# Performance work log

Hardware: AMD Instinct MI355X
Metric: run time of the kernel (lower is better)

Reference implementation:

```python
import jax, jax.numpy as jnp
import numpy as np

B, S, D = 2, 2048, 7168
R, H, VD = 1024, 16, 128
QK_HD = R // H            # 64, per-head latent q/k dim
SCALE = float(np.sqrt(D // H))  # self.scale = d_heads ** 0.5 = sqrt(448)


def setup_inputs() -> dict:
    key = jax.random.key(0)
    ks = jax.random.split(key, 6)
    return {
        "x":   jax.random.normal(ks[0], (B, S, D), dtype=jnp.float32),
        "Wq":  jax.random.normal(ks[1], (R, D), dtype=jnp.float32) * 0.02,
        "Wkv": jax.random.normal(ks[2], (R, D), dtype=jnp.float32) * 0.02,
        "Wvb": jax.random.normal(ks[3], (H * VD, R), dtype=jnp.float32) * 0.02,
        "Wo":  jax.random.normal(ks[4], (D, H * VD), dtype=jnp.float32) * 0.02,
        "bo":  jnp.zeros((D,), dtype=jnp.float32),
    }


def reference(x, Wq, Wkv, Wvb, Wo, bo):
    b, s, d = x.shape
    # low-rank compressed projections (torch Linear: y = x @ W.T)
    q_lat  = x @ Wq.T            # [B,S,R] compressed query
    kv_lat = x @ Wkv.T           # [B,S,R] compressed KV latent (shared K)
    q = q_lat.reshape(b, s, H, QK_HD)    # [B,S,H,64]
    k = kv_lat.reshape(b, s, H, QK_HD)   # [B,S,H,64]
    # up-project values from latent
    v = (kv_lat @ Wvb.T).reshape(b, s, H, VD)  # [B,S,H,128]
    # scaled causal attention in latent head space
    scores = jnp.einsum("bqhd,bkhd->bhqk", q, k) / SCALE  # [B,H,S,S]
    causal = jnp.tril(jnp.ones((s, s), dtype=bool))
    scores = jnp.where(causal, scores, jnp.finfo(scores.dtype).min)
    attn = jax.nn.softmax(scores, axis=-1)
    out = jnp.einsum("bhqk,bkhd->bqhd", attn, v).reshape(b, s, H * VD)
    return out @ Wo.T + bo       # [B,S,D]
```

## Files before the change

kernel.cpp:

```cpp
#include <hip/hip_runtime.h>
#include <hip/hip_bf16.h>

typedef __bf16 bf16_t;
typedef __attribute__((ext_vector_type(8))) __bf16 bf16x8;
typedef __attribute__((ext_vector_type(4))) __bf16 bf16x4;
typedef __attribute__((ext_vector_type(4))) float f32x4;

#define B_ 2
#define S_ 2048
#define D_ 7168
#define R_ 1024
#define H_ 16
#define VD_ 128
#define MROWS 4096
#define NQKV 2048
#define HVD 2048

__device__ __forceinline__ void gload_lds16(const bf16_t* g, bf16_t* l) {
    __builtin_amdgcn_global_load_lds(
        (const __attribute__((address_space(1))) unsigned int*)(g),
        (__attribute__((address_space(3))) unsigned int*)(l),
        16, 0, 0);
}

__global__ __launch_bounds__(256)
void cvt_f32_bf16(const float* __restrict__ src, bf16_t* __restrict__ dst, float scale) {
    size_t i = ((size_t)blockIdx.x * 256 + threadIdx.x) * 4;
    f32x4 v = *(const f32x4*)(src + i);
    bf16x4 o;
    o[0] = (bf16_t)(v[0] * scale);
    o[1] = (bf16_t)(v[1] * scale);
    o[2] = (bf16_t)(v[2] * scale);
    o[3] = (bf16_t)(v[3] * scale);
    *(bf16x4*)(dst + i) = o;
}

template<int OUTF32>
__global__ __launch_bounds__(256)
void gemm_bt(const bf16_t* __restrict__ A, int lda,
             const bf16_t* __restrict__ Bt, int ldb,
             void* __restrict__ Cv, int ldc,
             const float* __restrict__ bias, int K)
{
    __shared__ __align__(16) bf16_t As[128 * 64];
    __shared__ __align__(16) bf16_t Bs[128 * 64];
    const int tid  = threadIdx.x;
    const int lane = tid & 63;
    const int wave = tid >> 6;
    const int tileM = blockIdx.y * 128;
    const int tileN = blockIdx.x * 128;
    const int wr = (wave >> 1) * 64;
    const int wc = (wave & 1) * 64;
    const int r  = lane & 15;
    const int kq = lane >> 4;

    const bf16_t* Ag = A  + (size_t)tileM * lda;
    const bf16_t* Bg = Bt + (size_t)tileN * ldb;

    f32x4 acc[4][4] = {};

    for (int k0 = 0; k0 < K; k0 += 64) {
        #pragma unroll
        for (int i = 0; i < 4; ++i) {
            const int lin  = (i * 256 + tid) * 8;
            const int arow = lin >> 6;
            const int acol = (lin & 63) ^ ((arow & 7) << 3);
            gload_lds16(Ag + (size_t)arow * lda + k0 + acol, As + lin);
            gload_lds16(Bg + (size_t)arow * ldb + k0 + acol, Bs + lin);
        }
        __syncthreads();

        bf16x8 af[4][2], bfr[4][2];
        #pragma unroll
        for (int m = 0; m < 4; ++m)
            #pragma unroll
            for (int kk = 0; kk < 2; ++kk) {
                const int e = (wr + m * 16 + r) * 64 + kk * 32 + kq * 8;
                af[m][kk] = *(const bf16x8*)(As + (e ^ ((r & 7) << 3)));
            }
        #pragma unroll
        for (int n = 0; n < 4; ++n)
            #pragma unroll
            for (int kk = 0; kk < 2; ++kk) {
                const int e = (wc + n * 16 + r) * 64 + kk * 32 + kq * 8;
                bfr[n][kk] = *(const bf16x8*)(Bs + (e ^ ((r & 7) << 3)));
            }
        #pragma unroll
        for (int kk = 0; kk < 2; ++kk)
            #pragma unroll
            for (int m = 0; m < 4; ++m)
                #pragma unroll
                for (int n = 0; n < 4; ++n)
                    acc[m][n] = __builtin_amdgcn_mfma_f32_16x16x32_bf16(af[m][kk], bfr[n][kk], acc[m][n], 0, 0, 0);
        __syncthreads();
    }

    const int orow = tileM + wr + kq * 4;
    const int ocol = tileN + wc + r;
    if (OUTF32) {
        float* C = (float*)Cv;
        #pragma unroll
        for (int n = 0; n < 4; ++n) {
            float bv = bias[ocol + n * 16];
            #pragma unroll
            for (int m = 0; m < 4; ++m)
                #pragma unroll
                for (int j = 0; j < 4; ++j)
                    C[(size_t)(orow + m * 16 + j) * ldc + ocol + n * 16] = acc[m][n][j] + bv;
        }
    } else {
        bf16_t* C = (bf16_t*)Cv;
        #pragma unroll
        for (int m = 0; m < 4; ++m)
            #pragma unroll
            for (int n = 0; n < 4; ++n)
                #pragma unroll
                for (int j = 0; j < 4; ++j)
                    C[(size_t)(orow + m * 16 + j) * ldc + ocol + n * 16] = (bf16_t)acc[m][n][j];
    }
}

__device__ __forceinline__ void attn_qtile(
    const bf16_t* __restrict__ Q, const bf16_t* __restrict__ Kp,
    const bf16_t* __restrict__ Vp, bf16_t* __restrict__ Op,
    bf16_t* __restrict__ P_lds, int qbase, int lane)
{
    const int r  = lane & 15;
    const int kq = lane >> 4;

    bf16x8 qf[2][2];
    #pragma unroll
    for (int m = 0; m < 2; ++m)
        #pragma unroll
        for (int kk = 0; kk < 2; ++kk)
            qf[m][kk] = *(const bf16x8*)(Q + (size_t)(qbase + m * 16 + r) * NQKV + kk * 32 + kq * 8);

    f32x4 o[2][8] = {};
    float mst[2][4], lst[2][4];
    #pragma unroll
    for (int m = 0; m < 2; ++m)
        #pragma unroll
        for (int j = 0; j < 4; ++j) { mst[m][j] = -INFINITY; lst[m][j] = 0.0f; }

    const int nfull  = qbase >> 6;
    const int ntiles = (qbase + 95) >> 6;

    for (int t = 0; t < ntiles; ++t) {
        const int kvb = t * 64;
        f32x4 s[2][4] = {};
        #pragma unroll
        for (int n = 0; n < 4; ++n) {
            bf16x8 kf0 = *(const bf16x8*)(Kp + (size_t)(kvb + n * 16 + r) * NQKV + kq * 8);
            bf16x8 kf1 = *(const bf16x8*)(Kp + (size_t)(kvb + n * 16 + r) * NQKV + 32 + kq * 8);
            #pragma unroll
            for (int m = 0; m < 2; ++m) {
                s[m][n] = __builtin_amdgcn_mfma_f32_16x16x32_bf16(qf[m][0], kf0, s[m][n], 0, 0, 0);
                s[m][n] = __builtin_amdgcn_mfma_f32_16x16x32_bf16(qf[m][1], kf1, s[m][n], 0, 0, 0);
            }
        }
        if (t >= nfull) {
            #pragma unroll
            for (int m = 0; m < 2; ++m)
                #pragma unroll
                for (int n = 0; n < 4; ++n)
                    #pragma unroll
                    for (int j = 0; j < 4; ++j) {
                        int kc = kvb + n * 16 + r;
                        int qr = qbase + m * 16 + kq * 4 + j;
                        if (kc > qr) s[m][n][j] = -1e30f;
                    }
        }
        float mx[2][4];
        #pragma unroll
        for (int m = 0; m < 2; ++m)
            #pragma unroll
            for (int j = 0; j < 4; ++j) {
                float v = fmaxf(fmaxf(s[m][0][j], s[m][1][j]), fmaxf(s[m][2][j], s[m][3][j]));
                #pragma unroll
                for (int d = 1; d < 16; d <<= 1) v = fmaxf(v, __shfl_xor(v, d, 64));
                mx[m][j] = v;
            }
        bool need = false;
        #pragma unroll
        for (int m = 0; m < 2; ++m)
            #pragma unroll
            for (int j = 0; j < 4; ++j) need |= (mx[m][j] > mst[m][j] + 8.0f);
        if (__ballot(need)) {
            #pragma unroll
            for (int m = 0; m < 2; ++m)
                #pragma unroll
                for (int j = 0; j < 4; ++j) {
                    float mnew  = fmaxf(mst[m][j], mx[m][j]);
                    float alpha = __expf(mst[m][j] - mnew);
                    lst[m][j] *= alpha;
                    mst[m][j]  = mnew;
                    #pragma unroll
                    for (int n = 0; n < 8; ++n) o[m][n][j] *= alpha;
                }
        }
        #pragma unroll
        for (int m = 0; m < 2; ++m)
            #pragma unroll
            for (int j = 0; j < 4; ++j) {
                float rs = 0.0f;
                const int row = m * 16 + kq * 4 + j;
                #pragma unroll
                for (int n = 0; n < 4; ++n) {
                    float pv = __expf(s[m][n][j] - mst[m][j]);
                    rs += pv;
                    const int c = (n * 16 + r) ^ ((row & 7) << 3);
                    P_lds[row * 64 + c] = (bf16_t)pv;
                }
                #pragma unroll
                for (int d = 1; d < 16; d <<= 1) rs += __shfl_xor(rs, d, 64);
                lst[m][j] += rs;
            }
        __syncthreads();
        bf16x8 pf[2][2];
        #pragma unroll
        for (int m = 0; m < 2; ++m)
            #pragma unroll
            for (int kk = 0; kk < 2; ++kk) {
                const int e = (m * 16 + r) * 64 + kk * 32 + kq * 8;
                pf[m][kk] = *(const bf16x8*)(P_lds + (e ^ ((r & 7) << 3)));
            }
        #pragma unroll
        for (int n = 0; n < 8; ++n) {
            #pragma unroll
            for (int kk = 0; kk < 2; ++kk) {
                bf16x8 vf = *(const bf16x8*)(Vp + (size_t)(n * 16 + r) * MROWS + kvb + kk * 32 + kq * 8);
                #pragma unroll
                for (int m = 0; m < 2; ++m)
                    o[m][n] = __builtin_amdgcn_mfma_f32_16x16x32_bf16(pf[m][kk], vf, o[m][n], 0, 0, 0);
            }
        }
        __syncthreads();
    }

    #pragma unroll
    for (int m = 0; m < 2; ++m)
        #pragma unroll
        for (int j = 0; j < 4; ++j) {
            float inv = 1.0f / lst[m][j];
            int row = m * 16 + kq * 4 + j;
            #pragma unroll
            for (int n = 0; n < 8; ++n)
                Op[(size_t)(qbase + row) * HVD + n * 16 + r] = (bf16_t)(o[m][n][j] * inv);
        }
}

__global__ __launch_bounds__(64)
void attn_kernel(const bf16_t* __restrict__ qkv, const bf16_t* __restrict__ Vt,
                 bf16_t* __restrict__ O)
{
    __shared__ __align__(16) bf16_t P_lds[32 * 64];
    const int lane = threadIdx.x;
    const int p = blockIdx.x;
    const int h = blockIdx.y;
    const int b = blockIdx.z;

    const bf16_t* Q  = qkv + (size_t)(b * S_) * NQKV + h * 64;
    const bf16_t* Kp = qkv + (size_t)(b * S_) * NQKV + R_ + h * 64;
    const bf16_t* Vp = Vt + (size_t)(h * VD_) * MROWS + b * S_;
    bf16_t* Op = O + (size_t)(b * S_) * HVD + h * VD_;

    attn_qtile(Q, Kp, Vp, Op, P_lds, (63 - p) * 32, lane);
    attn_qtile(Q, Kp, Vp, Op, P_lds, p * 32, lane);
}

extern "C" void kernel_launch(void* const* d_in, const int* in_sizes, int n_in,
                              void* d_out, int out_size, void* d_ws, size_t ws_size,
                              hipStream_t stream) {
    const float* x   = (const float*)d_in[0];
    const float* Wq  = (const float*)d_in[1];
    const float* Wkv = (const float*)d_in[2];
    const float* Wvb = (const float*)d_in[3];
    const float* Wo  = (const float*)d_in[4];
    const float* bo  = (const float*)d_in[5];

    char* oc = (char*)d_out;
    bf16_t* xb     = (bf16_t*)oc;
    bf16_t* Wqkv_b = (bf16_t*)(oc + 58720256);
    char* ws = (char*)d_ws;
    bf16_t* qkv_b  = (bf16_t*)ws;
    bf16_t* Wvb_b  = (bf16_t*)(ws + 16777216);
    bf16_t* Vt_b   = (bf16_t*)(ws + 20971520);
    bf16_t* attn_b = (bf16_t*)(ws + 37748736);
    bf16_t* Wo_b   = (bf16_t*)(ws + 54525952);

    const float inv_scale = 0.047245559f;

    cvt_f32_bf16<<<29360128 / 1024, 256, 0, stream>>>(x,   xb, 1.0f);
    cvt_f32_bf16<<< 7340032 / 1024, 256, 0, stream>>>(Wq,  Wqkv_b, inv_scale);
    cvt_f32_bf16<<< 7340032 / 1024, 256, 0, stream>>>(Wkv, Wqkv_b + 7340032, 1.0f);
    cvt_f32_bf16<<< 2097152 / 1024, 256, 0, stream>>>(Wvb, Wvb_b, 1.0f);
    cvt_f32_bf16<<<14680064 / 1024, 256, 0, stream>>>(Wo,  Wo_b, 1.0f);

    gemm_bt<0><<<dim3(16, 32), 256, 0, stream>>>(xb, D_, Wqkv_b, D_, qkv_b, NQKV, nullptr, D_);
    gemm_bt<0><<<dim3(32, 16), 256, 0, stream>>>(Wvb_b, R_, qkv_b + R_, NQKV, Vt_b, MROWS, nullptr, R_);
    attn_kernel<<<dim3(32, H_, B_), 64, 0, stream>>>(qkv_b, Vt_b, attn_b);
    gemm_bt<1><<<dim3(56, 32), 256, 0, stream>>>(attn_b, HVD, Wo_b, HVD, d_out, D_, bo, HVD);
}
```

Before: 542.0 us.

## Double-buffer GEMM LDS tiles and split attention KV loop across four waves

```diff
diff --git a/kernel.cpp b/kernel.cpp
--- a/kernel.cpp
+++ b/kernel.cpp
@@ -42,8 +42,8 @@
              void* __restrict__ Cv, int ldc,
              const float* __restrict__ bias, int K)
 {
-    __shared__ __align__(16) bf16_t As[128 * 64];
-    __shared__ __align__(16) bf16_t Bs[128 * 64];
+    __shared__ __align__(16) bf16_t As[2][128 * 64];
+    __shared__ __align__(16) bf16_t Bs[2][128 * 64];
     const int tid  = threadIdx.x;
     const int lane = tid & 63;
     const int wave = tid >> 6;
@@ -57,18 +57,36 @@
     const bf16_t* Ag = A  + (size_t)tileM * lda;
     const bf16_t* Bg = Bt + (size_t)tileN * ldb;
 
+    int srow[4], scol[4], slin[4];
+    #pragma unroll
+    for (int i = 0; i < 4; ++i) {
+        slin[i] = (i * 256 + tid) * 8;
+        srow[i] = slin[i] >> 6;
+        scol[i] = (slin[i] & 63) ^ ((srow[i] & 7) << 3);
+    }
+
+    #define ISSUE_TILE(buf, k0)                                                  \
+        {                                                                        \
+            _Pragma("unroll")                                                    \
+            for (int i = 0; i < 4; ++i) {                                        \
+                gload_lds16(Ag + (size_t)srow[i] * lda + (k0) + scol[i], As[buf] + slin[i]); \
+                gload_lds16(Bg + (size_t)srow[i] * ldb + (k0) + scol[i], Bs[buf] + slin[i]); \
+            }                                                                    \
+        }
+
     f32x4 acc[4][4] = {};
-
-    for (int k0 = 0; k0 < K; k0 += 64) {
-        #pragma unroll
-        for (int i = 0; i < 4; ++i) {
-            const int lin  = (i * 256 + tid) * 8;
-            const int arow = lin >> 6;
-            const int acol = (lin & 63) ^ ((arow & 7) << 3);
-            gload_lds16(Ag + (size_t)arow * lda + k0 + acol, As + lin);
-            gload_lds16(Bg + (size_t)arow * ldb + k0 + acol, Bs + lin);
-        }
-        __syncthreads();
+    const int nt = K >> 6;
+
+    ISSUE_TILE(0, 0)
+    ISSUE_TILE(1, 64)
+    asm volatile("s_waitcnt vmcnt(8)" ::: "memory");
+    __builtin_amdgcn_s_barrier();
+    __builtin_amdgcn_sched_barrier(0);
+
+    for (int t = 0; t < nt; ++t) {
+        const int cur = t & 1;
+        const bf16_t* Ab = As[cur];
+        const bf16_t* Bb = Bs[cur];
 
         bf16x8 af[4][2], bfr[4][2];
         #pragma unroll
@@ -76,14 +94,14 @@
             #pragma unroll
             for (int kk = 0; kk < 2; ++kk) {
                 const int e = (wr + m * 16 + r) * 64 + kk * 32 + kq * 8;
-                af[m][kk] = *(const bf16x8*)(As + (e ^ ((r & 7) << 3)));
+                af[m][kk] = *(const bf16x8*)(Ab + (e ^ ((r & 7) << 3)));
             }
         #pragma unroll
         for (int n = 0; n < 4; ++n)
             #pragma unroll
             for (int kk = 0; kk < 2; ++kk) {
                 const int e = (wc + n * 16 + r) * 64 + kk * 32 + kq * 8;
-                bfr[n][kk] = *(const bf16x8*)(Bs + (e ^ ((r & 7) << 3)));
+                bfr[n][kk] = *(const bf16x8*)(Bb + (e ^ ((r & 7) << 3)));
             }
         #pragma unroll
         for (int kk = 0; kk < 2; ++kk)
@@ -92,8 +110,19 @@
                 #pragma unroll
                 for (int n = 0; n < 4; ++n)
                     acc[m][n] = __builtin_amdgcn_mfma_f32_16x16x32_bf16(af[m][kk], bfr[n][kk], acc[m][n], 0, 0, 0);
-        __syncthreads();
-    }
+
+        __builtin_amdgcn_s_barrier();
+        __builtin_amdgcn_sched_barrier(0);
+        if (t + 2 < nt) {
+            ISSUE_TILE(cur, (t + 2) << 6)
+            asm volatile("s_waitcnt vmcnt(8)" ::: "memory");
+        } else {
+            asm volatile("s_waitcnt vmcnt(0)" ::: "memory");
+        }
+        __builtin_amdgcn_s_barrier();
+        __builtin_amdgcn_sched_barrier(0);
+    }
+    #undef ISSUE_TILE
 
     const int orow = tileM + wr + kq * 4;
     const int ocol = tileN + wc + r;
@@ -120,10 +149,15 @@
     }
 }
 
-__device__ __forceinline__ void attn_qtile(
+#define OPAD 132
+
+__device__ __forceinline__ void attn_qtile32(
     const bf16_t* __restrict__ Q, const bf16_t* __restrict__ Kp,
     const bf16_t* __restrict__ Vp, bf16_t* __restrict__ Op,
-    bf16_t* __restrict__ P_lds, int qbase, int lane)
+    bf16_t* __restrict__ P_lds,
+    float* __restrict__ O_acc,
+    float* __restrict__ ml_m, float* __restrict__ ml_l,
+    int qbase, int wave, int lane, int tid)
 {
     const int r  = lane & 15;
     const int kq = lane >> 4;
@@ -145,7 +179,7 @@
     const int nfull  = qbase >> 6;
     const int ntiles = (qbase + 95) >> 6;
 
-    for (int t = 0; t < ntiles; ++t) {
+    for (int t = wave; t < ntiles; t += 4) {
         const int kvb = t * 64;
         f32x4 s[2][4] = {};
         #pragma unroll
@@ -215,7 +249,6 @@
                 for (int d = 1; d < 16; d <<= 1) rs += __shfl_xor(rs, d, 64);
                 lst[m][j] += rs;
             }
-        __syncthreads();
         bf16x8 pf[2][2];
         #pragma unroll
         for (int m = 0; m < 2; ++m)
@@ -234,27 +267,82 @@
                     o[m][n] = __builtin_amdgcn_mfma_f32_16x16x32_bf16(pf[m][kk], vf, o[m][n], 0, 0, 0);
             }
         }
+    }
+
+    if (r == 0) {
+        #pragma unroll
+        for (int m = 0; m < 2; ++m)
+            #pragma unroll
+            for (int j = 0; j < 4; ++j) {
+                const int row = m * 16 + kq * 4 + j;
+                ml_m[wave * 32 + row] = mst[m][j];
+                ml_l[wave * 32 + row] = lst[m][j];
+            }
+    }
+    __syncthreads();
+
+    float scl[2][4];
+    #pragma unroll
+    for (int m = 0; m < 2; ++m)
+        #pragma unroll
+        for (int j = 0; j < 4; ++j) {
+            const int row = m * 16 + kq * 4 + j;
+            float M = fmaxf(fmaxf(ml_m[0 * 32 + row], ml_m[1 * 32 + row]),
+                            fmaxf(ml_m[2 * 32 + row], ml_m[3 * 32 + row]));
+            scl[m][j] = __expf(mst[m][j] - M);
+        }
+
+    #pragma unroll
+    for (int wq = 0; wq < 4; ++wq) {
+        if (wave == wq) {
+            #pragma unroll
+            for (int m = 0; m < 2; ++m)
+                #pragma unroll
+                for (int n = 0; n < 8; ++n)
+                    #pragma unroll
+                    for (int j = 0; j < 4; ++j) {
+                        const int row = m * 16 + kq * 4 + j;
+                        const int idx = row * OPAD + n * 16 + r;
+                        float v = o[m][n][j] * scl[m][j];
+                        if (wq == 0) O_acc[idx] = v;
+                        else         O_acc[idx] += v;
+                    }
+        }
         __syncthreads();
     }
 
-    #pragma unroll
-    for (int m = 0; m < 2; ++m)
-        #pragma unroll
-        for (int j = 0; j < 4; ++j) {
-            float inv = 1.0f / lst[m][j];
-            int row = m * 16 + kq * 4 + j;
-            #pragma unroll
-            for (int n = 0; n < 8; ++n)
-                Op[(size_t)(qbase + row) * HVD + n * 16 + r] = (bf16_t)(o[m][n][j] * inv);
-        }
-}
-
-__global__ __launch_bounds__(64)
+    {
+        const int row = tid >> 3;
+        const int cg  = (tid & 7) * 16;
+        float M = fmaxf(fmaxf(ml_m[0 * 32 + row], ml_m[1 * 32 + row]),
+                        fmaxf(ml_m[2 * 32 + row], ml_m[3 * 32 + row]));
+        float lt = ml_l[0 * 32 + row] * __expf(ml_m[0 * 32 + row] - M)
+                 + ml_l[1 * 32 + row] * __expf(ml_m[1 * 32 + row] - M)
+                 + ml_l[2 * 32 + row] * __expf(ml_m[2 * 32 + row] - M)
+                 + ml_l[3 * 32 + row] * __expf(ml_m[3 * 32 + row] - M);
+        float inv = 1.0f / lt;
+        bf16x8 w0, w1;
+        #pragma unroll
+        for (int c = 0; c < 8; ++c) {
+            w0[c] = (bf16_t)(O_acc[row * OPAD + cg + c] * inv);
+            w1[c] = (bf16_t)(O_acc[row * OPAD + cg + 8 + c] * inv);
+        }
+        *(bf16x8*)(Op + (size_t)(qbase + row) * HVD + cg)     = w0;
+        *(bf16x8*)(Op + (size_t)(qbase + row) * HVD + cg + 8) = w1;
+    }
+    __syncthreads();
+}
+
+__global__ __launch_bounds__(256)
 void attn_kernel(const bf16_t* __restrict__ qkv, const bf16_t* __restrict__ Vt,
                  bf16_t* __restrict__ O)
 {
-    __shared__ __align__(16) bf16_t P_lds[32 * 64];
-    const int lane = threadIdx.x;
+    __shared__ __align__(16) bf16_t P_all[4][32 * 64];
+    __shared__ float O_acc[32 * OPAD];
+    __shared__ float ml_m[4 * 32], ml_l[4 * 32];
+    const int tid  = threadIdx.x;
+    const int lane = tid & 63;
+    const int wave = tid >> 6;
     const int p = blockIdx.x;
     const int h = blockIdx.y;
     const int b = blockIdx.z;
@@ -264,8 +352,10 @@
     const bf16_t* Vp = Vt + (size_t)(h * VD_) * MROWS + b * S_;
     bf16_t* Op = O + (size_t)(b * S_) * HVD + h * VD_;
 
-    attn_qtile(Q, Kp, Vp, Op, P_lds, (63 - p) * 32, lane);
-    attn_qtile(Q, Kp, Vp, Op, P_lds, p * 32, lane);
+    attn_qtile32(Q, Kp, Vp, Op, P_all[wave], O_acc, ml_m, ml_l,
+                 (63 - p) * 32, wave, lane, tid);
+    attn_qtile32(Q, Kp, Vp, Op, P_all[wave], O_acc, ml_m, ml_l,
+                 p * 32, wave, lane, tid);
 }
 
 extern "C" void kernel_launch(void* const* d_in, const int* in_sizes, int n_in,
@@ -298,6 +388,6 @@
 
     gemm_bt<0><<<dim3(16, 32), 256, 0, stream>>>(xb, D_, Wqkv_b, D_, qkv_b, NQKV, nullptr, D_);
     gemm_bt<0><<<dim3(32, 16), 256, 0, stream>>>(Wvb_b, R_, qkv_b + R_, NQKV, Vt_b, MROWS, nullptr, R_);
-    attn_kernel<<<dim3(32, H_, B_), 64, 0, stream>>>(qkv_b, Vt_b, attn_b);
+    attn_kernel<<<dim3(32, H_, B_), 256, 0, stream>>>(qkv_b, Vt_b, attn_b);
     gemm_bt<1><<<dim3(56, 32), 256, 0, stream>>>(attn_b, HVD, Wo_b, HVD, d_out, D_, bo, HVD);
 }
```

Measured after the change: 565.0 us. 4.2% more time.

## Double-buffer GEMM LDS tiles and prefetch K fragments in attention

Applied to the files above, without the earlier changes.

```diff
diff --git a/kernel.cpp b/kernel.cpp
--- a/kernel.cpp
+++ b/kernel.cpp
@@ -42,8 +42,8 @@
              void* __restrict__ Cv, int ldc,
              const float* __restrict__ bias, int K)
 {
-    __shared__ __align__(16) bf16_t As[128 * 64];
-    __shared__ __align__(16) bf16_t Bs[128 * 64];
+    __shared__ __align__(16) bf16_t As[2][128 * 64];
+    __shared__ __align__(16) bf16_t Bs[2][128 * 64];
     const int tid  = threadIdx.x;
     const int lane = tid & 63;
     const int wave = tid >> 6;
@@ -57,18 +57,36 @@
     const bf16_t* Ag = A  + (size_t)tileM * lda;
     const bf16_t* Bg = Bt + (size_t)tileN * ldb;
 
+    int srow[4], scol[4], slin[4];
+    #pragma unroll
+    for (int i = 0; i < 4; ++i) {
+        slin[i] = (i * 256 + tid) * 8;
+        srow[i] = slin[i] >> 6;
+        scol[i] = (slin[i] & 63) ^ ((srow[i] & 7) << 3);
+    }
+
+    #define ISSUE_TILE(buf, k0)                                                  \
+        {                                                                        \
+            _Pragma("unroll")                                                    \
+            for (int i = 0; i < 4; ++i) {                                        \
+                gload_lds16(Ag + (size_t)srow[i] * lda + (k0) + scol[i], As[buf] + slin[i]); \
+                gload_lds16(Bg + (size_t)srow[i] * ldb + (k0) + scol[i], Bs[buf] + slin[i]); \
+            }                                                                    \
+        }
+
     f32x4 acc[4][4] = {};
-
-    for (int k0 = 0; k0 < K; k0 += 64) {
-        #pragma unroll
-        for (int i = 0; i < 4; ++i) {
-            const int lin  = (i * 256 + tid) * 8;
-            const int arow = lin >> 6;
-            const int acol = (lin & 63) ^ ((arow & 7) << 3);
-            gload_lds16(Ag + (size_t)arow * lda + k0 + acol, As + lin);
-            gload_lds16(Bg + (size_t)arow * ldb + k0 + acol, Bs + lin);
-        }
-        __syncthreads();
+    const int nt = K >> 6;
+
+    ISSUE_TILE(0, 0)
+    ISSUE_TILE(1, 64)
+    asm volatile("s_waitcnt vmcnt(8)" ::: "memory");
+    __builtin_amdgcn_s_barrier();
+    __builtin_amdgcn_sched_barrier(0);
+
+    for (int t = 0; t < nt; ++t) {
+        const int cur = t & 1;
+        const bf16_t* Ab = As[cur];
+        const bf16_t* Bb = Bs[cur];
 
         bf16x8 af[4][2], bfr[4][2];
         #pragma unroll
@@ -76,14 +94,14 @@
             #pragma unroll
             for (int kk = 0; kk < 2; ++kk) {
                 const int e = (wr + m * 16 + r) * 64 + kk * 32 + kq * 8;
-                af[m][kk] = *(const bf16x8*)(As + (e ^ ((r & 7) << 3)));
+                af[m][kk] = *(const bf16x8*)(Ab + (e ^ ((r & 7) << 3)));
             }
         #pragma unroll
         for (int n = 0; n < 4; ++n)
             #pragma unroll
             for (int kk = 0; kk < 2; ++kk) {
                 const int e = (wc + n * 16 + r) * 64 + kk * 32 + kq * 8;
-                bfr[n][kk] = *(const bf16x8*)(Bs + (e ^ ((r & 7) << 3)));
+                bfr[n][kk] = *(const bf16x8*)(Bb + (e ^ ((r & 7) << 3)));
             }
         #pragma unroll
         for (int kk = 0; kk < 2; ++kk)
@@ -92,8 +110,19 @@
                 #pragma unroll
                 for (int n = 0; n < 4; ++n)
                     acc[m][n] = __builtin_amdgcn_mfma_f32_16x16x32_bf16(af[m][kk], bfr[n][kk], acc[m][n], 0, 0, 0);
-        __syncthreads();
-    }
+
+        __builtin_amdgcn_s_barrier();
+        __builtin_amdgcn_sched_barrier(0);
+        if (t + 2 < nt) {
+            ISSUE_TILE(cur, (t + 2) << 6)
+            asm volatile("s_waitcnt vmcnt(8)" ::: "memory");
+        } else {
+            asm volatile("s_waitcnt vmcnt(0)" ::: "memory");
+        }
+        __builtin_amdgcn_s_barrier();
+        __builtin_amdgcn_sched_barrier(0);
+    }
+    #undef ISSUE_TILE
 
     const int orow = tileM + wr + kq * 4;
     const int ocol = tileN + wc + r;
@@ -120,7 +149,28 @@
     }
 }
 
-__device__ __forceinline__ void attn_qtile(
+#define LOADK(KF, kvb_)                                                          \
+    {                                                                            \
+        _Pragma("unroll")                                                        \
+        for (int n = 0; n < 4; ++n) {                                            \
+            const bf16_t* kp_ = Kp + (size_t)((kvb_) + n * 16 + r) * NQKV + kq * 8; \
+            KF[n][0] = *(const bf16x8*)kp_;                                      \
+            KF[n][1] = *(const bf16x8*)(kp_ + 32);                               \
+        }                                                                        \
+    }
+
+#define QKMM(KF)                                                                 \
+    {                                                                            \
+        _Pragma("unroll")                                                        \
+        for (int n = 0; n < 4; ++n)                                              \
+            _Pragma("unroll")                                                    \
+            for (int m = 0; m < 2; ++m) {                                        \
+                s[m][n] = __builtin_amdgcn_mfma_f32_16x16x32_bf16(qf[m][0], KF[n][0], s[m][n], 0, 0, 0); \
+                s[m][n] = __builtin_amdgcn_mfma_f32_16x16x32_bf16(qf[m][1], KF[n][1], s[m][n], 0, 0, 0); \
+            }                                                                    \
+    }
+
+__device__ __forceinline__ void attn_qtile32(
     const bf16_t* __restrict__ Q, const bf16_t* __restrict__ Kp,
     const bf16_t* __restrict__ Vp, bf16_t* __restrict__ Op,
     bf16_t* __restrict__ P_lds, int qbase, int lane)
@@ -145,18 +195,17 @@
     const int nfull  = qbase >> 6;
     const int ntiles = (qbase + 95) >> 6;
 
+    bf16x8 kfA[4][2], kfB[4][2];
+    LOADK(kfA, 0)
+
     for (int t = 0; t < ntiles; ++t) {
         const int kvb = t * 64;
+        const bool useA = ((t & 1) == 0);
         f32x4 s[2][4] = {};
-        #pragma unroll
-        for (int n = 0; n < 4; ++n) {
-            bf16x8 kf0 = *(const bf16x8*)(Kp + (size_t)(kvb + n * 16 + r) * NQKV + kq * 8);
-            bf16x8 kf1 = *(const bf16x8*)(Kp + (size_t)(kvb + n * 16 + r) * NQKV + 32 + kq * 8);
-            #pragma unroll
-            for (int m = 0; m < 2; ++m) {
-                s[m][n] = __builtin_amdgcn_mfma_f32_16x16x32_bf16(qf[m][0], kf0, s[m][n], 0, 0, 0);
-                s[m][n] = __builtin_amdgcn_mfma_f32_16x16x32_bf16(qf[m][1], kf1, s[m][n], 0, 0, 0);
-            }
+        if (useA) { QKMM(kfA) } else { QKMM(kfB) }
+        if (t + 1 < ntiles) {
+            const int nk = (t + 1) * 64;
+            if (useA) { LOADK(kfB, nk) } else { LOADK(kfA, nk) }
         }
         if (t >= nfull) {
             #pragma unroll
@@ -215,7 +264,6 @@
                 for (int d = 1; d < 16; d <<= 1) rs += __shfl_xor(rs, d, 64);
                 lst[m][j] += rs;
             }
-        __syncthreads();
         bf16x8 pf[2][2];
         #pragma unroll
         for (int m = 0; m < 2; ++m)
@@ -234,7 +282,6 @@
                     o[m][n] = __builtin_amdgcn_mfma_f32_16x16x32_bf16(pf[m][kk], vf, o[m][n], 0, 0, 0);
             }
         }
-        __syncthreads();
     }
 
     #pragma unroll
@@ -249,7 +296,7 @@
         }
 }
 
-__global__ __launch_bounds__(64)
+__global__ __launch_bounds__(64, 1)
 void attn_kernel(const bf16_t* __restrict__ qkv, const bf16_t* __restrict__ Vt,
                  bf16_t* __restrict__ O)
 {
@@ -264,8 +311,8 @@
     const bf16_t* Vp = Vt + (size_t)(h * VD_) * MROWS + b * S_;
     bf16_t* Op = O + (size_t)(b * S_) * HVD + h * VD_;
 
-    attn_qtile(Q, Kp, Vp, Op, P_lds, (63 - p) * 32, lane);
-    attn_qtile(Q, Kp, Vp, Op, P_lds, p * 32, lane);
+    attn_qtile32(Q, Kp, Vp, Op, P_lds, (63 - p) * 32, lane);
+    attn_qtile32(Q, Kp, Vp, Op, P_lds, p * 32, lane);
 }
 
 extern "C" void kernel_launch(void* const* d_in, const int* in_sizes, int n_in,
```

New measurement: 602.1 us. 11.1% more time.
